# Optimization experiments

Hardware: AMD Instinct MI355X
Metric: run time of the kernel (lower is better)

The kernel has to match this reference:

```python
import jax, jax.numpy as jnp
import numpy as np

# patch sizes are (width, height) pairs, matching the torch zip unpack
PATCHES = [(54, 30), (27, 15), (18, 10), (9, 5)]
D_MODEL = 256
B, T, H, W = 2, 4, 120, 216


def setup_inputs() -> dict:
    key = jax.random.key(0)
    ks = jax.random.split(key, 10)
    bt = B * T
    x = jax.random.normal(ks[0], (bt, D_MODEL, H, W), jnp.float32)
    m = jax.random.uniform(ks[1], (bt, 1, H, W), dtype=jnp.float32)
    s1 = 1.0 / np.sqrt(D_MODEL).astype(np.float32)
    Wq = jax.random.normal(ks[2], (D_MODEL, D_MODEL), jnp.float32) * s1
    bq = jnp.zeros((D_MODEL,), jnp.float32)
    Wk = jax.random.normal(ks[3], (D_MODEL, D_MODEL), jnp.float32) * s1
    bk = jnp.zeros((D_MODEL,), jnp.float32)
    Wv = jax.random.normal(ks[4], (D_MODEL, D_MODEL), jnp.float32) * s1
    bv = jnp.zeros((D_MODEL,), jnp.float32)
    s3 = 1.0 / np.sqrt(D_MODEL * 9).astype(np.float32)
    Wo = jax.random.normal(ks[5], (D_MODEL, D_MODEL, 3, 3), jnp.float32) * s3
    bo = jnp.zeros((D_MODEL,), jnp.float32)
    return dict(x=x, m=m, Wq=Wq, bq=bq, Wk=Wk, bk=bk, Wv=Wv, bv=bv,
                Wo=Wo, bo=bo, b=B, c=D_MODEL)


def _patchify(v, b, t, dk, oh, hh, ow, ww):
    # (b*t, dk, h, w) -> (b, t*oh*ow, dk*hh*ww)
    v = v.reshape(b, t, dk, oh, hh, ow, ww)
    v = v.transpose(0, 1, 3, 5, 2, 4, 6)
    return v.reshape(b, t * oh * ow, dk * hh * ww)


def _forward(x, m, Wq, bq, Wk, bk, Wv, bv, Wo, bo, b, c):
    bt, _, h, w = x.shape
    t = bt // b
    dk = c // len(PATCHES)
    q = jnp.einsum('bchw,oc->bohw', x, Wq) + bq[None, :, None, None]
    k = jnp.einsum('bchw,oc->bohw', x, Wk) + bk[None, :, None, None]
    v = jnp.einsum('bchw,oc->bohw', x, Wv) + bv[None, :, None, None]
    outs = []
    for i, (pw, ph) in enumerate(PATCHES):
        ow, oh = w // pw, h // ph
        sl = slice(i * dk, (i + 1) * dk)
        qi = _patchify(q[:, sl], b, t, dk, oh, ph, ow, pw)
        ki = _patchify(k[:, sl], b, t, dk, oh, ph, ow, pw)
        vi = _patchify(v[:, sl], b, t, dk, oh, ph, ow, pw)
        # mask: mean over each patch > 0.5, broadcast over query tokens
        mm = m.reshape(b, t, 1, oh, ph, ow, pw).transpose(0, 1, 3, 5, 2, 4, 6)
        mm = mm.reshape(b, t * oh * ow, ph * pw)
        mask = (jnp.mean(mm, axis=-1) > 0.5)[:, None, :]  # (b, 1, N)
        d = qi.shape[-1]
        scores = jnp.einsum('bnd,bmd->bnm', qi, ki) / jnp.sqrt(jnp.float32(d))
        scores = jnp.where(mask, jnp.float32(-1e9), scores)
        p = jax.nn.softmax(scores, axis=-1)
        yi = jnp.einsum('bnm,bmd->bnd', p, vi)
        yi = yi.reshape(b, t, oh, ow, dk, ph, pw)
        yi = yi.transpose(0, 1, 4, 2, 5, 3, 6).reshape(bt, dk, h, w)
        outs.append(yi)
    y = jnp.concatenate(outs, axis=1)  # (bt, c, h, w)
    out = jax.lax.conv_general_dilated(y, Wo, (1, 1), 'SAME',
                                       dimension_numbers=('NCHW', 'OIHW', 'NCHW'))
    out = out + bo[None, :, None, None]
    return jnp.where(out >= 0, out, 0.2 * out)  # LeakyReLU(0.2)


def reference(x, m, Wq, bq, Wk, bk, Wv, bv, Wo, bo, b, c):
    return _forward(x, m, Wq, bq, Wk, bk, Wv, bv, Wo, bo, b, c)
```

## Files before the change

kernel.cpp:

```cpp
#include <hip/hip_runtime.h>
#include <hip/hip_bf16.h>
#include <math.h>

typedef __hip_bfloat16 bf16;
typedef __attribute__((ext_vector_type(8))) short short8v;
typedef __attribute__((ext_vector_type(4))) float floatx4;

#define TT 4
#define CCH 256
#define HGT 120
#define WID 216
#define HWP (HGT*WID)
#define NBT 8

__device__ __forceinline__ float bfu2f(unsigned short u) {
    union { unsigned int i; float f; } c; c.i = ((unsigned int)u) << 16; return c.f;
}
__device__ __forceinline__ unsigned short f2bu(float f) {
    bf16 h = __float2bfloat16(f);
    return *(unsigned short*)&h;
}
__device__ __forceinline__ short8v lds_load8(const unsigned short* p) {
    short8v r;
    *(uint2*)&r       = *(const uint2*)p;
    *((uint2*)&r + 1) = *(const uint2*)(p + 4);
    return r;
}

__global__ __launch_bounds__(256)
void wqkv_prep_kernel(const float* __restrict__ Wq, const float* __restrict__ Wk,
                      const float* __restrict__ Wv, unsigned short* __restrict__ wqkv)
{
    int idx = blockIdx.x*256 + threadIdx.x;
    int kind = idx >> 16;
    int rem = idx & 65535;
    const float* src = (kind == 0) ? Wq : (kind == 1) ? Wk : Wv;
    wqkv[idx] = f2bu(src[rem]);
}

__global__ __launch_bounds__(256)
void qkv_mfma_kernel(const float* __restrict__ x, const unsigned short* __restrict__ wqkv,
                     const float* __restrict__ bq, const float* __restrict__ bk,
                     const float* __restrict__ bv,
                     unsigned short* __restrict__ Qp, unsigned short* __restrict__ Kp,
                     unsigned short* __restrict__ Vt,
                     int c0, int oh, int ow, int ph, int pw, int N, int D)
{
    __shared__ unsigned short xs[64*36];
    __shared__ unsigned short wl[3*64*36];
    const int tid = threadIdx.x;
    const int bt = blockIdx.y;
    const int p0 = blockIdx.x * 64;
    const int b = bt / TT, t = bt % TT;
    const int lane = tid & 63, wv = tid >> 6;
    const int col = lane & 15, kg = lane >> 4;
    const int phalf = wv & 1, ohalf = wv >> 1;

    floatx4 acc[3][2][2];
    #pragma unroll
    for (int kk = 0; kk < 3; ++kk)
        #pragma unroll
        for (int og = 0; og < 2; ++og)
            #pragma unroll
            for (int pg = 0; pg < 2; ++pg)
                acc[kk][og][pg] = (floatx4){0.f,0.f,0.f,0.f};

    const int spx = tid & 63, scg = tid >> 6;
    const int so = tid >> 2, swg = tid & 3;

    for (int cb = 0; cb < CCH; cb += 32) {
        __syncthreads();
        {
            const float* xp = x + ((size_t)bt*CCH + cb + scg*8)*HWP + p0 + spx;
            unsigned short tmp[8];
            #pragma unroll
            for (int j = 0; j < 8; ++j) tmp[j] = f2bu(xp[(size_t)j*HWP]);
            uint2* dst = (uint2*)&xs[spx*36 + scg*8];
            dst[0] = make_uint2((unsigned)tmp[0] | ((unsigned)tmp[1]<<16),
                                (unsigned)tmp[2] | ((unsigned)tmp[3]<<16));
            dst[1] = make_uint2((unsigned)tmp[4] | ((unsigned)tmp[5]<<16),
                                (unsigned)tmp[6] | ((unsigned)tmp[7]<<16));
        }
        #pragma unroll
        for (int kk = 0; kk < 3; ++kk) {
            uint4 w4 = *(const uint4*)(wqkv + ((size_t)(kk*256 + c0 + so))*256 + cb + swg*8);
            uint2* dst = (uint2*)&wl[kk*2304 + so*36 + swg*8];
            dst[0] = make_uint2(w4.x, w4.y);
            dst[1] = make_uint2(w4.z, w4.w);
        }
        __syncthreads();
        short8v bx[2];
        #pragma unroll
        for (int pg = 0; pg < 2; ++pg)
            bx[pg] = lds_load8(&xs[(phalf*32 + pg*16 + col)*36 + kg*8]);
        #pragma unroll
        for (int kk = 0; kk < 3; ++kk) {
            #pragma unroll
            for (int og = 0; og < 2; ++og) {
                short8v aw = lds_load8(&wl[kk*2304 + (ohalf*32 + og*16 + col)*36 + kg*8]);
                #pragma unroll
                for (int pg = 0; pg < 2; ++pg)
                    acc[kk][og][pg] = __builtin_amdgcn_mfma_f32_16x16x32_bf16(
                        aw, bx[pg], acc[kk][og][pg], 0, 0, 0);
            }
        }
    }

    const int phpw = ph*pw;
    #pragma unroll
    for (int pg = 0; pg < 2; ++pg) {
        const int p = p0 + phalf*32 + pg*16 + col;
        const int h = p / WID, w = p - h*WID;
        const int ohi = h / ph, py = h - ohi*ph;
        const int owi = w / pw, pxx = w - owi*pw;
        const int n = (t*oh + ohi)*ow + owi;
        const int doff = py*pw + pxx;
        const size_t rbase = ((size_t)b*N + n)*(size_t)D;
        #pragma unroll
        for (int og = 0; og < 2; ++og) {
            #pragma unroll
            for (int r = 0; r < 4; ++r) {
                const int ck = ohalf*32 + og*16 + kg*4 + r;
                const int d = ck*phpw + doff;
                Qp[rbase + d] = f2bu(acc[0][og][pg][r] + bq[c0+ck]);
                Kp[rbase + d] = f2bu(acc[1][og][pg][r] + bk[c0+ck]);
                Vt[((size_t)b*D + d)*N + n] = f2bu(acc[2][og][pg][r] + bv[c0+ck]);
            }
        }
    }
}

__global__ __launch_bounds__(256)
void mask_kernel(const float* __restrict__ m, float* __restrict__ maskf,
                 int oh, int ow, int ph, int pw, int N)
{
    const int bn = blockIdx.x;
    const int b = bn / N, n = bn % N;
    const int ohow = oh*ow;
    const int t = n / ohow, r = n % ohow;
    const int ohi = r / ow, owi = r % ow;
    const float* mp = m + (size_t)(b*TT + t)*HWP;
    const int cnt = ph*pw;
    double s = 0.0;
    for (int i = threadIdx.x; i < cnt; i += 256) {
        int py = i / pw, px = i % pw;
        s += (double)mp[(size_t)(ohi*ph + py)*WID + owi*pw + px];
    }
    __shared__ double red[4];
    #pragma unroll
    for (int off = 32; off > 0; off >>= 1) s += __shfl_down(s, off);
    if ((threadIdx.x & 63) == 0) red[threadIdx.x >> 6] = s;
    __syncthreads();
    if (threadIdx.x == 0) {
        double tot = red[0]+red[1]+red[2]+red[3];
        maskf[bn] = (tot > 0.5*(double)cnt) ? 1.0f : 0.0f;
    }
}

__global__ void zero_kernel(float* __restrict__ p, int n) {
    int i = blockIdx.x*256 + threadIdx.x;
    if (i < n) p[i] = 0.f;
}

__global__ __launch_bounds__(256)
void scores_mfma_kernel(const unsigned short* __restrict__ Qp,
                        const unsigned short* __restrict__ Kp,
                        float* __restrict__ S, int N, int D, int nsplit)
{
    __shared__ unsigned short qs[64*36], ks[64*36];
    const int tid = threadIdx.x;
    const int b = blockIdx.z / nsplit, sp = blockIdx.z % nsplit;
    const int kchunks = D >> 5;
    const int per = (kchunks + nsplit - 1) / nsplit;
    const int k0 = sp*per*32;
    const int k1 = min(D, k0 + per*32);
    const unsigned short* Qb = Qp + (size_t)b*N*D;
    const unsigned short* Kb = Kp + (size_t)b*N*D;
    const int n0 = blockIdx.y*64, m0 = blockIdx.x*64;
    const int lane = tid & 63, wv = tid >> 6;
    const int col = lane & 15, kg = lane >> 4;
    const int nhalf = wv & 1, mhalf = wv >> 1;
    const int stok = tid >> 2, sgg = tid & 3;

    floatx4 acc[2][2];
    #pragma unroll
    for (int i = 0; i < 2; ++i)
        #pragma unroll
        for (int j = 0; j < 2; ++j) acc[i][j] = (floatx4){0.f,0.f,0.f,0.f};

    for (int kb = k0; kb < k1; kb += 32) {
        __syncthreads();
        {
            uint4 q4 = *(const uint4*)(Qb + (size_t)(n0+stok)*D + kb + sgg*8);
            uint2* qd = (uint2*)&qs[stok*36 + sgg*8];
            qd[0] = make_uint2(q4.x, q4.y); qd[1] = make_uint2(q4.z, q4.w);
            uint4 k4 = *(const uint4*)(Kb + (size_t)(m0+stok)*D + kb + sgg*8);
            uint2* kd = (uint2*)&ks[stok*36 + sgg*8];
            kd[0] = make_uint2(k4.x, k4.y); kd[1] = make_uint2(k4.z, k4.w);
        }
        __syncthreads();
        short8v aq[2], bk2[2];
        #pragma unroll
        for (int i = 0; i < 2; ++i)
            aq[i] = lds_load8(&qs[(nhalf*32 + i*16 + col)*36 + kg*8]);
        #pragma unroll
        for (int j = 0; j < 2; ++j)
            bk2[j] = lds_load8(&ks[(mhalf*32 + j*16 + col)*36 + kg*8]);
        #pragma unroll
        for (int i = 0; i < 2; ++i)
            #pragma unroll
            for (int j = 0; j < 2; ++j)
                acc[i][j] = __builtin_amdgcn_mfma_f32_16x16x32_bf16(
                    aq[i], bk2[j], acc[i][j], 0, 0, 0);
    }
    #pragma unroll
    for (int i = 0; i < 2; ++i) {
        #pragma unroll
        for (int j = 0; j < 2; ++j) {
            #pragma unroll
            for (int r = 0; r < 4; ++r) {
                const int n = n0 + nhalf*32 + i*16 + kg*4 + r;
                const int mm = m0 + mhalf*32 + j*16 + col;
                const size_t a = ((size_t)b*N + n)*N + mm;
                if (nsplit > 1) atomicAdd(&S[a], acc[i][j][r]);
                else            S[a] = acc[i][j][r];
            }
        }
    }
}

__global__ __launch_bounds__(256)
void softmax_kernel(const float* __restrict__ S, const float* __restrict__ maskf,
                    unsigned short* __restrict__ Pout, int N, float rscale)
{
    __shared__ float buf[2304];
    __shared__ float red[4];
    __shared__ float bval;
    const int tid = threadIdx.x;
    const int bn = blockIdx.x;
    const int b = bn / N;
    const float* rowp = S + (size_t)bn*N;
    const float* mk = maskf + (size_t)b*N;
    float mx = -3.0e38f;
    for (int mc = tid; mc < N; mc += 256) {
        float s = rowp[mc]*rscale;
        if (mk[mc] > 0.5f) s = -1e9f;
        buf[mc] = s;
        mx = fmaxf(mx, s);
    }
    #pragma unroll
    for (int off = 32; off > 0; off >>= 1) mx = fmaxf(mx, __shfl_down(mx, off));
    if ((tid & 63) == 0) red[tid >> 6] = mx;
    __syncthreads();
    if (tid == 0) bval = fmaxf(fmaxf(red[0],red[1]), fmaxf(red[2],red[3]));
    __syncthreads();
    const float rm = bval;
    float sum = 0.f;
    for (int mc = tid; mc < N; mc += 256) {
        float e = __expf(buf[mc]-rm);
        buf[mc] = e; sum += e;
    }
    #pragma unroll
    for (int off = 32; off > 0; off >>= 1) sum += __shfl_down(sum, off);
    if ((tid & 63) == 0) red[tid >> 6] = sum;
    __syncthreads();
    if (tid == 0) bval = 1.0f/(red[0]+red[1]+red[2]+red[3]);
    __syncthreads();
    const float inv = bval;
    unsigned short* prow = Pout + (size_t)bn*N;
    for (int mc = tid; mc < N; mc += 256) prow[mc] = f2bu(buf[mc]*inv);
}

__global__ __launch_bounds__(256)
void pv_mfma_kernel(const unsigned short* __restrict__ Pb, const unsigned short* __restrict__ Vt,
                    unsigned short* __restrict__ y, int N, int D,
                    int c0, int oh, int ow, int ph, int pw)
{
    __shared__ unsigned short ps[64*36], vs[64*36];
    const int tid = threadIdx.x;
    const int b = blockIdx.z;
    const unsigned short* Pbb = Pb + (size_t)b*N*N;
    const unsigned short* Vbb = Vt + (size_t)b*D*N;
    const int n0 = blockIdx.y*64, d0 = blockIdx.x*64;
    const int lane = tid & 63, wv = tid >> 6;
    const int col = lane & 15, kg = lane >> 4;
    const int nhalf = wv & 1, dhalf = wv >> 1;
    const int stok = tid >> 2, sgg = tid & 3;

    floatx4 acc[2][2];
    #pragma unroll
    for (int i = 0; i < 2; ++i)
        #pragma unroll
        for (int j = 0; j < 2; ++j) acc[i][j] = (floatx4){0.f,0.f,0.f,0.f};

    for (int mb = 0; mb < N; mb += 32) {
        __syncthreads();
        {
            uint4 p4 = *(const uint4*)(Pbb + (size_t)(n0+stok)*N + mb + sgg*8);
            uint2* pd = (uint2*)&ps[stok*36 + sgg*8];
            pd[0] = make_uint2(p4.x, p4.y); pd[1] = make_uint2(p4.z, p4.w);
            uint4 v4 = *(const uint4*)(Vbb + (size_t)(d0+stok)*N + mb + sgg*8);
            uint2* vd = (uint2*)&vs[stok*36 + sgg*8];
            vd[0] = make_uint2(v4.x, v4.y); vd[1] = make_uint2(v4.z, v4.w);
        }
        __syncthreads();
        short8v ap[2], bv2[2];
        #pragma unroll
        for (int i = 0; i < 2; ++i)
            ap[i] = lds_load8(&ps[(nhalf*32 + i*16 + col)*36 + kg*8]);
        #pragma unroll
        for (int j = 0; j < 2; ++j)
            bv2[j] = lds_load8(&vs[(dhalf*32 + j*16 + col)*36 + kg*8]);
        #pragma unroll
        for (int i = 0; i < 2; ++i)
            #pragma unroll
            for (int j = 0; j < 2; ++j)
                acc[i][j] = __builtin_amdgcn_mfma_f32_16x16x32_bf16(
                    ap[i], bv2[j], acc[i][j], 0, 0, 0);
    }

    const int ohow = oh*ow, phpw = ph*pw;
    #pragma unroll
    for (int j = 0; j < 2; ++j) {
        const int d = d0 + dhalf*32 + j*16 + col;
        const int ck = d / phpw, r2 = d - ck*phpw;
        const int py = r2 / pw, pxx = r2 - py*pw;
        #pragma unroll
        for (int i = 0; i < 2; ++i) {
            #pragma unroll
            for (int r = 0; r < 4; ++r) {
                const int n = n0 + nhalf*32 + i*16 + kg*4 + r;
                const int t = n / ohow, rn = n - t*ohow;
                const int ohi = rn / ow, owi = rn - ohi*ow;
                y[((size_t)(b*TT + t)*CCH + c0 + ck)*HWP +
                  (size_t)(ohi*ph + py)*WID + owi*pw + pxx] = f2bu(acc[i][j][r]);
            }
        }
    }
}

__global__ __launch_bounds__(256)
void wprep_kernel(const float* __restrict__ Wo, bf16* __restrict__ wbf)
{
    int i = blockIdx.x*256 + threadIdx.x;
    int o = i >> 8, c = i & 255;
    const float* src = Wo + (size_t)(o*256 + c)*9;
    #pragma unroll
    for (int off = 0; off < 9; ++off)
        wbf[(size_t)(off*256 + o)*256 + c] = __float2bfloat16(src[off]);
}

__global__ __launch_bounds__(256)
void conv_mfma_kernel(const bf16* __restrict__ y, const bf16* __restrict__ wbf,
                      const float* __restrict__ bo, float* __restrict__ out)
{
    __shared__ unsigned short ys[108*36];
    __shared__ unsigned short wl[9*64*36];
    const int tid = threadIdx.x;
    const int bz = blockIdx.z;
    const int bt = bz >> 2, o0 = (bz & 3) * 64;
    const int w0 = blockIdx.x * 16, h0 = blockIdx.y * 4;
    const int lane = tid & 63, wv = tid >> 6;
    const int col = lane & 15, kg = lane >> 4;
    const int phalf = wv & 1, ohalf = wv >> 1;

    floatx4 acc[2][2];
    #pragma unroll
    for (int pg = 0; pg < 2; ++pg)
        #pragma unroll
        for (int og = 0; og < 2; ++og)
            acc[pg][og] = (floatx4){0.f, 0.f, 0.f, 0.f};

    const unsigned short* yu = (const unsigned short*)y;
    const unsigned short* wu = (const unsigned short*)wbf;
    const int so = tid >> 2, scg = tid & 3;

    for (int cb = 0; cb < CCH; cb += 32) {
        __syncthreads();
        for (int i = tid; i < 3456; i += 256) {
            int c = i / 108, pos = i - c*108;
            int ry = pos / 18, rx = pos - ry*18;
            int gh = h0 - 1 + ry, gw = w0 - 1 + rx;
            unsigned short v = 0;
            if (gh >= 0 && gh < HGT && gw >= 0 && gw < WID)
                v = yu[((size_t)bt*CCH + cb + c)*HWP + (size_t)gh*WID + gw];
            ys[pos*36 + c] = v;
        }
        #pragma unroll
        for (int off = 0; off < 9; ++off) {
            uint4 w4 = *(const uint4*)(wu + ((size_t)(off*256 + o0 + so)*256 + cb + scg*8));
            uint2* dst = (uint2*)&wl[off*2304 + so*36 + scg*8];
            dst[0] = make_uint2(w4.x, w4.y);
            dst[1] = make_uint2(w4.z, w4.w);
        }
        __syncthreads();
        #pragma unroll
        for (int off = 0; off < 9; ++off) {
            const int ky = off / 3, kx = off - ky*3;
            short8v aw[2], by[2];
            #pragma unroll
            for (int og = 0; og < 2; ++og)
                aw[og] = lds_load8(&wl[off*2304 + (ohalf*32 + og*16 + col)*36 + kg*8]);
            #pragma unroll
            for (int pg = 0; pg < 2; ++pg) {
                const int py = phalf*2 + pg;
                by[pg] = lds_load8(&ys[((py + ky)*18 + col + kx)*36 + kg*8]);
            }
            #pragma unroll
            for (int pg = 0; pg < 2; ++pg)
                #pragma unroll
                for (int og = 0; og < 2; ++og)
                    acc[pg][og] = __builtin_amdgcn_mfma_f32_16x16x32_bf16(
                        aw[og], by[pg], acc[pg][og], 0, 0, 0);
        }
    }

    const int gw = w0 + col;
    if (gw < WID) {
        #pragma unroll
        for (int pg = 0; pg < 2; ++pg) {
            const int py = phalf*2 + pg;
            #pragma unroll
            for (int og = 0; og < 2; ++og) {
                #pragma unroll
                for (int r = 0; r < 4; ++r) {
                    int o = o0 + ohalf*32 + og*16 + kg*4 + r;
                    float vr = acc[pg][og][r] + bo[o];
                    out[((size_t)bt*CCH + o)*HWP + (size_t)(h0 + py)*WID + gw] =
                        (vr >= 0.f) ? vr : 0.2f*vr;
                }
            }
        }
    }
}

extern "C" void kernel_launch(void* const* d_in, const int* in_sizes, int n_in,
                              void* d_out, int out_size, void* d_ws, size_t ws_size,
                              hipStream_t stream)
{
    const float* x  = (const float*)d_in[0];
    const float* m  = (const float*)d_in[1];
    const float* Wq = (const float*)d_in[2];
    const float* bq = (const float*)d_in[3];
    const float* Wk = (const float*)d_in[4];
    const float* bk = (const float*)d_in[5];
    const float* Wv = (const float*)d_in[6];
    const float* bv = (const float*)d_in[7];
    const float* Wo = (const float*)d_in[8];
    const float* bo = (const float*)d_in[9];
    float* out = (float*)d_out;

    char* ws = (char*)d_ws;
    unsigned short* Qp = (unsigned short*)(ws + 0);
    unsigned short* Kp = (unsigned short*)(ws + 26542080);
    unsigned short* Vt = (unsigned short*)(ws + 53084160);
    float* S  = (float*)(ws + 79626240);
    bf16*  Y  = (bf16*) (ws + 122093568);
    float* MK = (float*)(ws + 228261888);
    unsigned short* WQKV = (unsigned short*)(ws + 228280320);
    unsigned short* Pb16 = Qp;
    bf16*  WB = (bf16*)(ws + 0);

    static const int s_pw[4] = {54,27,18,9};
    static const int s_ph[4] = {30,15,10,5};
    static const int s_oo[4] = {4,8,12,24};
    static const int s_N[4]  = {64,256,576,2304};
    static const int s_D[4]  = {103680,25920,11520,2880};
    static const int s_sp[4] = {256,64,16,1};

    wqkv_prep_kernel<<<dim3(768), 256, 0, stream>>>(Wq, Wk, Wv, WQKV);

    for (int s = 0; s < 4; ++s) {
        const int pw = s_pw[s], ph = s_ph[s], oo = s_oo[s];
        const int N = s_N[s], D = s_D[s], nsplit = s_sp[s];
        const int c0 = s*64;
        qkv_mfma_kernel<<<dim3(405, NBT), 256, 0, stream>>>(
            x, WQKV, bq, bk, bv, Qp, Kp, Vt, c0, oo, oo, ph, pw, N, D);
        mask_kernel<<<dim3(2*N), 256, 0, stream>>>(m, MK, oo, oo, ph, pw, N);
        if (nsplit > 1) {
            const int ztot = 2*N*N;
            zero_kernel<<<dim3((ztot+255)/256), 256, 0, stream>>>(S, ztot);
        }
        scores_mfma_kernel<<<dim3(N/64, N/64, 2*nsplit), 256, 0, stream>>>(Qp, Kp, S, N, D, nsplit);
        softmax_kernel<<<dim3(2*N), 256, 0, stream>>>(S, MK, Pb16, N, 1.0f/sqrtf((float)D));
        pv_mfma_kernel<<<dim3(D/64, N/64, 2), 256, 0, stream>>>(
            Pb16, Vt, (unsigned short*)Y, N, D, c0, oo, oo, ph, pw);
    }
    wprep_kernel<<<dim3(256), 256, 0, stream>>>(Wo, WB);
    conv_mfma_kernel<<<dim3(14, 30, NBT*4), 256, 0, stream>>>(Y, WB, bo, out);
}
```

Before: 3.085 ms.

## Store attention output channels-last and enlarge conv tiles for vectorized loads

The PV kernel now writes the intermediate attention output in NHWC layout (channel innermost) instead of NCHW. This lets the 3x3 conv kernel load 8 contiguous channels per 16-byte vector instead of gathering scalar bf16 values. The conv tile also doubles in each spatial dimension (32x8 pixels, all 64 output channels per wave) with a 4x4 accumulator grid, which raises weight reuse and MFMA density per LDS load. In exchange, the PV kernel's scattered 2-byte stores become strided by 256 channels, register pressure and LDS use in the conv grow, and the conv launches fewer blocks.

Result: faster. 2.792 ms (-9.5%).

```diff
diff --git a/kernel.cpp b/kernel.cpp
--- a/kernel.cpp
+++ b/kernel.cpp
@@ -273,7 +273,7 @@
 
 __global__ __launch_bounds__(256)
 void pv_mfma_kernel(const unsigned short* __restrict__ Pb, const unsigned short* __restrict__ Vt,
-                    unsigned short* __restrict__ y, int N, int D,
+                    unsigned short* __restrict__ y2, int N, int D,
                     int c0, int oh, int ow, int ph, int pw)
 {
     __shared__ unsigned short ps[64*36], vs[64*36];
@@ -332,8 +332,8 @@
                 const int n = n0 + nhalf*32 + i*16 + kg*4 + r;
                 const int t = n / ohow, rn = n - t*ohow;
                 const int ohi = rn / ow, owi = rn - ohi*ow;
-                y[((size_t)(b*TT + t)*CCH + c0 + ck)*HWP +
-                  (size_t)(ohi*ph + py)*WID + owi*pw + pxx] = f2bu(acc[i][j][r]);
+                y2[((size_t)(b*TT + t)*HWP + (size_t)(ohi*ph + py)*WID + owi*pw + pxx)*CCH
+                   + c0 + ck] = f2bu(acc[i][j][r]);
             }
         }
     }
@@ -351,45 +351,51 @@
 }
 
 __global__ __launch_bounds__(256)
-void conv_mfma_kernel(const bf16* __restrict__ y, const bf16* __restrict__ wbf,
+void conv_mfma_kernel(const unsigned short* __restrict__ y2, const bf16* __restrict__ wbf,
                       const float* __restrict__ bo, float* __restrict__ out)
 {
-    __shared__ unsigned short ys[108*36];
+    __shared__ unsigned short ys[340*36];
     __shared__ unsigned short wl[9*64*36];
     const int tid = threadIdx.x;
     const int bz = blockIdx.z;
     const int bt = bz >> 2, o0 = (bz & 3) * 64;
-    const int w0 = blockIdx.x * 16, h0 = blockIdx.y * 4;
+    const int w0 = blockIdx.x * 32, h0 = blockIdx.y * 8;
     const int lane = tid & 63, wv = tid >> 6;
     const int col = lane & 15, kg = lane >> 4;
-    const int phalf = wv & 1, ohalf = wv >> 1;
-
-    floatx4 acc[2][2];
-    #pragma unroll
-    for (int pg = 0; pg < 2; ++pg)
-        #pragma unroll
-        for (int og = 0; og < 2; ++og)
+    const int py0 = wv * 2;
+
+    floatx4 acc[4][4];
+    #pragma unroll
+    for (int pg = 0; pg < 4; ++pg)
+        #pragma unroll
+        for (int og = 0; og < 4; ++og)
             acc[pg][og] = (floatx4){0.f, 0.f, 0.f, 0.f};
 
-    const unsigned short* yu = (const unsigned short*)y;
     const unsigned short* wu = (const unsigned short*)wbf;
-    const int so = tid >> 2, scg = tid & 3;
+    const int so = tid >> 2, swg = tid & 3;
 
     for (int cb = 0; cb < CCH; cb += 32) {
         __syncthreads();
-        for (int i = tid; i < 3456; i += 256) {
-            int c = i / 108, pos = i - c*108;
-            int ry = pos / 18, rx = pos - ry*18;
-            int gh = h0 - 1 + ry, gw = w0 - 1 + rx;
-            unsigned short v = 0;
-            if (gh >= 0 && gh < HGT && gw >= 0 && gw < WID)
-                v = yu[((size_t)bt*CCH + cb + c)*HWP + (size_t)gh*WID + gw];
-            ys[pos*36 + c] = v;
+        #pragma unroll
+        for (int k = 0; k < 6; ++k) {
+            int idx = tid + k*256;
+            if (idx < 1360) {
+                int pos = idx >> 2, q = idx & 3;
+                int ry = pos / 34, rx = pos - ry*34;
+                int gh = h0 - 1 + ry, gw = w0 - 1 + rx;
+                uint4 v = make_uint4(0,0,0,0);
+                if (gh >= 0 && gh < HGT && gw >= 0 && gw < WID)
+                    v = *(const uint4*)(y2 + (((size_t)bt*HWP + (size_t)gh*WID + gw)<<8)
+                                        + cb + q*8);
+                uint2* dst = (uint2*)&ys[pos*36 + q*8];
+                dst[0] = make_uint2(v.x, v.y);
+                dst[1] = make_uint2(v.z, v.w);
+            }
         }
         #pragma unroll
         for (int off = 0; off < 9; ++off) {
-            uint4 w4 = *(const uint4*)(wu + ((size_t)(off*256 + o0 + so)*256 + cb + scg*8));
-            uint2* dst = (uint2*)&wl[off*2304 + so*36 + scg*8];
+            uint4 w4 = *(const uint4*)(wu + ((size_t)(off*256 + o0 + so)*256 + cb + swg*8));
+            uint2* dst = (uint2*)&wl[off*2304 + so*36 + swg*8];
             dst[0] = make_uint2(w4.x, w4.y);
             dst[1] = make_uint2(w4.z, w4.w);
         }
@@ -397,36 +403,37 @@
         #pragma unroll
         for (int off = 0; off < 9; ++off) {
             const int ky = off / 3, kx = off - ky*3;
-            short8v aw[2], by[2];
-            #pragma unroll
-            for (int og = 0; og < 2; ++og)
-                aw[og] = lds_load8(&wl[off*2304 + (ohalf*32 + og*16 + col)*36 + kg*8]);
-            #pragma unroll
-            for (int pg = 0; pg < 2; ++pg) {
-                const int py = phalf*2 + pg;
-                by[pg] = lds_load8(&ys[((py + ky)*18 + col + kx)*36 + kg*8]);
-            }
-            #pragma unroll
-            for (int pg = 0; pg < 2; ++pg)
+            short8v aw[4], by[4];
+            #pragma unroll
+            for (int og = 0; og < 4; ++og)
+                aw[og] = lds_load8(&wl[off*2304 + (og*16 + col)*36 + kg*8]);
+            #pragma unroll
+            for (int pg = 0; pg < 4; ++pg) {
+                const int ry = py0 + (pg >> 1) + ky;
+                const int rx = (pg & 1)*16 + col + kx;
+                by[pg] = lds_load8(&ys[(ry*34 + rx)*36 + kg*8]);
+            }
+            #pragma unroll
+            for (int pg = 0; pg < 4; ++pg)
                 #pragma unroll
-                for (int og = 0; og < 2; ++og)
+                for (int og = 0; og < 4; ++og)
                     acc[pg][og] = __builtin_amdgcn_mfma_f32_16x16x32_bf16(
                         aw[og], by[pg], acc[pg][og], 0, 0, 0);
         }
     }
 
-    const int gw = w0 + col;
-    if (gw < WID) {
-        #pragma unroll
-        for (int pg = 0; pg < 2; ++pg) {
-            const int py = phalf*2 + pg;
-            #pragma unroll
-            for (int og = 0; og < 2; ++og) {
+    #pragma unroll
+    for (int pg = 0; pg < 4; ++pg) {
+        const int gh = h0 + py0 + (pg >> 1);
+        const int gw = w0 + (pg & 1)*16 + col;
+        if (gw < WID) {
+            #pragma unroll
+            for (int og = 0; og < 4; ++og) {
                 #pragma unroll
                 for (int r = 0; r < 4; ++r) {
-                    int o = o0 + ohalf*32 + og*16 + kg*4 + r;
+                    int o = o0 + og*16 + kg*4 + r;
                     float vr = acc[pg][og][r] + bo[o];
-                    out[((size_t)bt*CCH + o)*HWP + (size_t)(h0 + py)*WID + gw] =
+                    out[((size_t)bt*CCH + o)*HWP + (size_t)gh*WID + gw] =
                         (vr >= 0.f) ? vr : 0.2f*vr;
                 }
             }
@@ -455,7 +462,7 @@
     unsigned short* Kp = (unsigned short*)(ws + 26542080);
     unsigned short* Vt = (unsigned short*)(ws + 53084160);
     float* S  = (float*)(ws + 79626240);
-    bf16*  Y  = (bf16*) (ws + 122093568);
+    unsigned short* Y2 = (unsigned short*)(ws + 122093568);
     float* MK = (float*)(ws + 228261888);
     unsigned short* WQKV = (unsigned short*)(ws + 228280320);
     unsigned short* Pb16 = Qp;
@@ -484,8 +491,8 @@
         scores_mfma_kernel<<<dim3(N/64, N/64, 2*nsplit), 256, 0, stream>>>(Qp, Kp, S, N, D, nsplit);
         softmax_kernel<<<dim3(2*N), 256, 0, stream>>>(S, MK, Pb16, N, 1.0f/sqrtf((float)D));
         pv_mfma_kernel<<<dim3(D/64, N/64, 2), 256, 0, stream>>>(
-            Pb16, Vt, (unsigned short*)Y, N, D, c0, oo, oo, ph, pw);
+            Pb16, Vt, Y2, N, D, c0, oo, oo, ph, pw);
     }
     wprep_kernel<<<dim3(256), 256, 0, stream>>>(Wo, WB);
-    conv_mfma_kernel<<<dim3(14, 30, NBT*4), 256, 0, stream>>>(Y, WB, bo, out);
-}
+    conv_mfma_kernel<<<dim3(7, 15, NBT*4), 256, 0, stream>>>(Y2, WB, bo, out);
+}
```
